# Kernel optimization log

Hardware: AMD Instinct MI355X
Metric: run time of the kernel (lower is better)

## Reference

```python
import jax, jax.numpy as jnp
import numpy as np

IN_SHAPE = 8192
OUT_SHAPE = 32
BATCH = 16384


def setup_inputs() -> dict:
    key = jax.random.key(0)
    kx, kw = jax.random.split(key)
    x = jax.random.normal(kx, (BATCH, IN_SHAPE), dtype=jnp.float32)
    # matches torch init: (rand*2-1)*0.001 -> uniform(-0.001, 0.001)
    weight = jax.random.uniform(kw, (OUT_SHAPE, IN_SHAPE), dtype=jnp.float32,
                                minval=-0.001, maxval=0.001)
    return {"x": x, "weight": weight}


def _binarize(weight):
    # scale = mean(|W|), detached
    scale = jax.lax.stop_gradient(jnp.mean(jnp.abs(weight)))
    clipped = jnp.clip(weight, -1.0, 1.0)
    # STE: forward value = scale*sign(W); gradient flows through clipped W
    return jax.lax.stop_gradient(scale * jnp.sign(weight) - clipped) + clipped


def reference(x, weight):
    bw = _binarize(weight)            # [out, in]
    return x @ bw.T                   # [batch, out]
```

## Files before the change

### kernel.cpp

```cpp
#include <hip/hip_runtime.h>

#define BATCH 16384
#define KDIM  8192
#define ODIM  32
#define SK    8
#define KSLICE (KDIM / SK)
#define KHALF  (KSLICE / 2)
#define KT    32
#define NT    (KHALF / KT)
#define THREADS 256

typedef short bf16x8 __attribute__((ext_vector_type(8)));
typedef float f32x16 __attribute__((ext_vector_type(16)));

__global__ void prep_kernel(const float* __restrict__ w,
                            unsigned short* __restrict__ bwTo,
                            float* __restrict__ partial) {
    int idx = blockIdx.x * 256 + threadIdx.x;
    float v = w[idx];
    bwTo[idx] = (v > 0.f) ? 0x3F80u : ((v < 0.f) ? 0xBF80u : 0u);

    float a = fabsf(v);
    #pragma unroll
    for (int off = 32; off; off >>= 1) a += __shfl_down(a, off, 64);
    __shared__ float red[4];
    int lane = threadIdx.x & 63, wv = threadIdx.x >> 6;
    if (lane == 0) red[wv] = a;
    __syncthreads();
    if (threadIdx.x == 0)
        partial[blockIdx.x] = (red[0] + red[1]) + (red[2] + red[3]);
}

__global__ __launch_bounds__(THREADS, 6)
void main_kernel(const float* __restrict__ x,
                 const unsigned short* __restrict__ bwTo,
                 float* __restrict__ pout) {
    __shared__ union {
        float buf[4][2][32][KT];
        float part[2][64][33];
    } sm;

    const int tid  = threadIdx.x;
    const int wv   = __builtin_amdgcn_readfirstlane(tid >> 6);
    const int lane = tid & 63;
    const int l31  = lane & 31, lhi = lane >> 5;
    const int kH   = wv & 1;
    const int rH   = wv >> 1;
    const int kb   = blockIdx.x & 7;
    const int rb   = blockIdx.x >> 3;
    const size_t rowbase = (size_t)rb * 64;
    const int kbase = kb * KSLICE + kH * KHALF;

    const int srow8 = lane >> 3;
    const int sc    = lane & 7;
    const int ssl   = sc ^ srow8;
    const float* __restrict__ g0 =
        x + (rowbase + rH * 32 + srow8) * (size_t)KDIM + kbase + 4 * sc;
    const float* __restrict__ g1 = g0 + (size_t)8  * KDIM;
    const float* __restrict__ g2 = g0 + (size_t)16 * KDIM;
    const float* __restrict__ g3 = g0 + (size_t)24 * KDIM;

    const unsigned short* __restrict__ bp =
        bwTo + (size_t)l31 * KDIM + kbase + lhi * 8;

    const int m7 = l31 & 7;
    const int ro00 = 4 * ((0 + 2 * lhi) ^ m7);
    const int ro01 = 4 * ((1 + 2 * lhi) ^ m7);
    const int ro10 = 4 * ((4 + 2 * lhi) ^ m7);
    const int ro11 = 4 * ((5 + 2 * lhi) ^ m7);
    const float* const rb0 = &sm.buf[wv][0][l31][0];
    const float* const rb1 = &sm.buf[wv][1][l31][0];

    f32x16 acc;
    #pragma unroll
    for (int i = 0; i < 16; ++i) acc[i] = 0.f;

    float4 st0, st1, st2, st3;
#define LOADT(t) do {                               \
        st0 = *(const float4*)(g0 + (t) * KT);      \
        st1 = *(const float4*)(g1 + (t) * KT);      \
        st2 = *(const float4*)(g2 + (t) * KT);      \
        st3 = *(const float4*)(g3 + (t) * KT);      \
    } while (0)
#define WRITET(db) do {                                         \
        *(float4*)&sm.buf[wv][db][srow8     ][4 * ssl] = st0;   \
        *(float4*)&sm.buf[wv][db][srow8 +  8][4 * ssl] = st1;   \
        *(float4*)&sm.buf[wv][db][srow8 + 16][4 * ssl] = st2;   \
        *(float4*)&sm.buf[wv][db][srow8 + 24][4 * ssl] = st3;   \
    } while (0)

    bf16x8 ahi, alo;
#define STEP(base, o0, o1, bfr) do {                                      \
        const float4 xa = *(const float4*)((base) + (o0));                \
        const float4 xb = *(const float4*)((base) + (o1));                \
        const float xf[8] = {xa.x, xa.y, xa.z, xa.w,                      \
                             xb.x, xb.y, xb.z, xb.w};                     \
        _Pragma("unroll")                                                 \
        for (int j = 0; j < 8; ++j) {                                     \
            unsigned bu = __float_as_uint(xf[j]);                         \
            float lo = xf[j] - __uint_as_float(bu & 0xFFFF0000u);         \
            ahi[j] = (short)(bu >> 16);                                   \
            alo[j] = (short)(__float_as_uint(lo) >> 16);                  \
        }                                                                 \
        acc = __builtin_amdgcn_mfma_f32_32x32x16_bf16(ahi, bfr, acc, 0, 0, 0); \
        acc = __builtin_amdgcn_mfma_f32_32x32x16_bf16(alo, bfr, acc, 0, 0, 0); \
    } while (0)

    LOADT(0);
    WRITET(0);
    LOADT(1);
    bf16x8 b0 = *(const bf16x8*)(bp);
    bf16x8 b1 = *(const bf16x8*)(bp + 16);

    for (int t = 0; t < NT; ++t) {
        const int db = t & 1;
        const float* base = db ? rb1 : rb0;

        STEP(base, ro00, ro01, b0);

        bf16x8 bn0, bn1;
        if (t + 1 < NT) {
            bn0 = *(const bf16x8*)(bp + (t + 1) * KT);
            bn1 = *(const bf16x8*)(bp + (t + 1) * KT + 16);
        }

        STEP(base, ro10, ro11, b1);

        if (t + 1 < NT) WRITET(db ^ 1);
        if (t + 2 < NT) LOADT(t + 2);
        b0 = bn0; b1 = bn1;
    }
#undef LOADT
#undef WRITET
#undef STEP

    __syncthreads();
    #pragma unroll
    for (int r = 0; r < 16; ++r) {
        int row32 = (r & 3) + 8 * (r >> 2) + 4 * lhi;
        sm.part[kH][rH * 32 + row32][l31] = acc[r];
    }
    __syncthreads();

    float* __restrict__ pb = pout + ((size_t)kb * BATCH + rowbase) * ODIM;
    #pragma unroll
    for (int i = 0; i < 8; ++i) {
        int j = tid + THREADS * i;
        int r = j >> 5, o = j & 31;
        pb[j] = sm.part[0][r][o] + sm.part[1][r][o];
    }
}

__global__ void reduce_kernel(const float* __restrict__ pout,
                              const float* __restrict__ partial,
                              float* __restrict__ out) {
    const int t = threadIdx.x;
    float a = (partial[t] + partial[t + 256]) + (partial[t + 512] + partial[t + 768]);
    #pragma unroll
    for (int off = 32; off; off >>= 1) a += __shfl_down(a, off, 64);
    __shared__ float red[4];
    __shared__ float sbc;
    if ((t & 63) == 0) red[t >> 6] = a;
    __syncthreads();
    if (t == 0)
        sbc = ((red[0] + red[1]) + (red[2] + red[3])) / (float)(ODIM * KDIM);
    __syncthreads();
    const float s = sbc;

    const int STRIDE = BATCH * ODIM / 4;
    int i = blockIdx.x * 256 + t;
    const float4* p = (const float4*)pout;
    float4 r = p[i];
    #pragma unroll
    for (int k = 1; k < SK; ++k) {
        float4 A = p[i + k * STRIDE];
        r.x += A.x; r.y += A.y; r.z += A.z; r.w += A.w;
    }
    r.x *= s; r.y *= s; r.z *= s; r.w *= s;
    ((float4*)out)[i] = r;
}

extern "C" void kernel_launch(void* const* d_in, const int* in_sizes, int n_in,
                              void* d_out, int out_size, void* d_ws, size_t ws_size,
                              hipStream_t stream) {
    const float* x = (const float*)d_in[0];
    const float* w = (const float*)d_in[1];
    float* out = (float*)d_out;

    float* wsf = (float*)d_ws;
    float* partial       = wsf;
    unsigned short* bwTo = (unsigned short*)(wsf + 1024);
    float* pout          = wsf + 1024 + (ODIM * KDIM / 2);

    prep_kernel<<<1024, 256, 0, stream>>>(w, bwTo, partial);
    main_kernel<<<256 * SK, THREADS, 0, stream>>>(x, bwTo, pout);
    reduce_kernel<<<BATCH * ODIM / 4 / 256, 256, 0, stream>>>(pout, partial, out);
}
```

Baseline: 126.5 us.

## Round x to single bf16 at load, store bf16 tiles in LDS, widen K tile

Replaces the split hi/lo bf16 emulation of fp32 (two MFMAs per step) with a single round-to-nearest bf16 conversion done at global-load time, so LDS holds bf16 instead of fp32 and each step issues one MFMA. The K tile doubles to 64 with a new swizzle, the B fragments are loaded directly per step rather than prefetched, and launch bounds drop to 5 waves. This halves MFMA work and LDS traffic but cuts x precision to bf16, which may break accuracy tolerance against the fp32 reference.

```diff
diff --git a/kernel.cpp b/kernel.cpp
--- a/kernel.cpp
+++ b/kernel.cpp
@@ -6,12 +6,21 @@
 #define SK    8
 #define KSLICE (KDIM / SK)
 #define KHALF  (KSLICE / 2)
-#define KT    32
+#define KT    64
 #define NT    (KHALF / KT)
 #define THREADS 256
 
 typedef short bf16x8 __attribute__((ext_vector_type(8)));
 typedef float f32x16 __attribute__((ext_vector_type(16)));
+
+__device__ __forceinline__ uint2 pack_bf16rn(float4 v) {
+    unsigned b0 = __float_as_uint(v.x), b1 = __float_as_uint(v.y);
+    unsigned b2 = __float_as_uint(v.z), b3 = __float_as_uint(v.w);
+    uint2 r;
+    r.x = ((b0 + 0x8000u) >> 16) | ((b1 + 0x8000u) & 0xFFFF0000u);
+    r.y = ((b2 + 0x8000u) >> 16) | ((b3 + 0x8000u) & 0xFFFF0000u);
+    return r;
+}
 
 __global__ void prep_kernel(const float* __restrict__ w,
                             unsigned short* __restrict__ bwTo,
@@ -31,12 +40,12 @@
         partial[blockIdx.x] = (red[0] + red[1]) + (red[2] + red[3]);
 }
 
-__global__ __launch_bounds__(THREADS, 6)
+__global__ __launch_bounds__(THREADS, 5)
 void main_kernel(const float* __restrict__ x,
                  const unsigned short* __restrict__ bwTo,
                  float* __restrict__ pout) {
     __shared__ union {
-        float buf[4][2][32][KT];
+        unsigned short buf[4][2][32][KT];
         float part[2][64][33];
     } sm;
 
@@ -44,6 +53,7 @@
     const int wv   = __builtin_amdgcn_readfirstlane(tid >> 6);
     const int lane = tid & 63;
     const int l31  = lane & 31, lhi = lane >> 5;
+    const int m7   = l31 & 7;
     const int kH   = wv & 1;
     const int rH   = wv >> 1;
     const int kb   = blockIdx.x & 7;
@@ -51,86 +61,77 @@
     const size_t rowbase = (size_t)rb * 64;
     const int kbase = kb * KSLICE + kH * KHALF;
 
-    const int srow8 = lane >> 3;
-    const int sc    = lane & 7;
-    const int ssl   = sc ^ srow8;
-    const float* __restrict__ g0 =
-        x + (rowbase + rH * 32 + srow8) * (size_t)KDIM + kbase + 4 * sc;
-    const float* __restrict__ g1 = g0 + (size_t)8  * KDIM;
-    const float* __restrict__ g2 = g0 + (size_t)16 * KDIM;
-    const float* __restrict__ g3 = g0 + (size_t)24 * KDIM;
+    const int srow4 = lane >> 4;
+    const int sc    = lane & 15;
+    const float* __restrict__ gb =
+        x + (rowbase + rH * 32 + srow4) * (size_t)KDIM + kbase + 4 * sc;
+
+    const int chE = (((sc >> 1) ^ srow4) << 3) + (sc & 1) * 4;
+    const int chO = chE ^ 32;
 
     const unsigned short* __restrict__ bp =
         bwTo + (size_t)l31 * KDIM + kbase + lhi * 8;
 
-    const int m7 = l31 & 7;
-    const int ro00 = 4 * ((0 + 2 * lhi) ^ m7);
-    const int ro01 = 4 * ((1 + 2 * lhi) ^ m7);
-    const int ro10 = 4 * ((4 + 2 * lhi) ^ m7);
-    const int ro11 = 4 * ((5 + 2 * lhi) ^ m7);
-    const float* const rb0 = &sm.buf[wv][0][l31][0];
-    const float* const rb1 = &sm.buf[wv][1][l31][0];
+    const int ro0 = l31 * 64 + (((0 + lhi) ^ m7) << 3);
+    const int ro1 = l31 * 64 + (((2 + lhi) ^ m7) << 3);
+    const int ro2 = l31 * 64 + (((4 + lhi) ^ m7) << 3);
+    const int ro3 = l31 * 64 + (((6 + lhi) ^ m7) << 3);
+    const unsigned short* const rbA = &sm.buf[wv][0][0][0];
+    const unsigned short* const rbB = &sm.buf[wv][1][0][0];
 
     f32x16 acc;
     #pragma unroll
     for (int i = 0; i < 16; ++i) acc[i] = 0.f;
 
-    float4 st0, st1, st2, st3;
-#define LOADT(t) do {                               \
-        st0 = *(const float4*)(g0 + (t) * KT);      \
-        st1 = *(const float4*)(g1 + (t) * KT);      \
-        st2 = *(const float4*)(g2 + (t) * KT);      \
-        st3 = *(const float4*)(g3 + (t) * KT);      \
-    } while (0)
-#define WRITET(db) do {                                         \
-        *(float4*)&sm.buf[wv][db][srow8     ][4 * ssl] = st0;   \
-        *(float4*)&sm.buf[wv][db][srow8 +  8][4 * ssl] = st1;   \
-        *(float4*)&sm.buf[wv][db][srow8 + 16][4 * ssl] = st2;   \
-        *(float4*)&sm.buf[wv][db][srow8 + 24][4 * ssl] = st3;   \
+    uint2 pk0, pk1, pk2, pk3, pk4, pk5, pk6, pk7;
+
+#define LOADPACK(t) do {                                                      \
+        float4 s0 = *(const float4*)(gb + (size_t) 0 * KDIM + (t) * KT);      \
+        float4 s1 = *(const float4*)(gb + (size_t) 4 * KDIM + (t) * KT);      \
+        float4 s2 = *(const float4*)(gb + (size_t) 8 * KDIM + (t) * KT);      \
+        float4 s3 = *(const float4*)(gb + (size_t)12 * KDIM + (t) * KT);      \
+        pk0 = pack_bf16rn(s0); pk1 = pack_bf16rn(s1);                         \
+        pk2 = pack_bf16rn(s2); pk3 = pack_bf16rn(s3);                         \
+        float4 s4 = *(const float4*)(gb + (size_t)16 * KDIM + (t) * KT);      \
+        float4 s5 = *(const float4*)(gb + (size_t)20 * KDIM + (t) * KT);      \
+        float4 s6 = *(const float4*)(gb + (size_t)24 * KDIM + (t) * KT);      \
+        float4 s7 = *(const float4*)(gb + (size_t)28 * KDIM + (t) * KT);      \
+        pk4 = pack_bf16rn(s4); pk5 = pack_bf16rn(s5);                         \
+        pk6 = pack_bf16rn(s6); pk7 = pack_bf16rn(s7);                         \
     } while (0)
 
-    bf16x8 ahi, alo;
-#define STEP(base, o0, o1, bfr) do {                                      \
-        const float4 xa = *(const float4*)((base) + (o0));                \
-        const float4 xb = *(const float4*)((base) + (o1));                \
-        const float xf[8] = {xa.x, xa.y, xa.z, xa.w,                      \
-                             xb.x, xb.y, xb.z, xb.w};                     \
-        _Pragma("unroll")                                                 \
-        for (int j = 0; j < 8; ++j) {                                     \
-            unsigned bu = __float_as_uint(xf[j]);                         \
-            float lo = xf[j] - __uint_as_float(bu & 0xFFFF0000u);         \
-            ahi[j] = (short)(bu >> 16);                                   \
-            alo[j] = (short)(__float_as_uint(lo) >> 16);                  \
-        }                                                                 \
-        acc = __builtin_amdgcn_mfma_f32_32x32x16_bf16(ahi, bfr, acc, 0, 0, 0); \
-        acc = __builtin_amdgcn_mfma_f32_32x32x16_bf16(alo, bfr, acc, 0, 0, 0); \
+#define WRITET(db) do {                                                       \
+        *(uint2*)&sm.buf[wv][db][ 0 + srow4][chE] = pk0;                      \
+        *(uint2*)&sm.buf[wv][db][ 4 + srow4][chO] = pk1;                      \
+        *(uint2*)&sm.buf[wv][db][ 8 + srow4][chE] = pk2;                      \
+        *(uint2*)&sm.buf[wv][db][12 + srow4][chO] = pk3;                      \
+        *(uint2*)&sm.buf[wv][db][16 + srow4][chE] = pk4;                      \
+        *(uint2*)&sm.buf[wv][db][20 + srow4][chO] = pk5;                      \
+        *(uint2*)&sm.buf[wv][db][24 + srow4][chE] = pk6;                      \
+        *(uint2*)&sm.buf[wv][db][28 + srow4][chO] = pk7;                      \
     } while (0)
 
-    LOADT(0);
+#define STEP(base, ro, boff) do {                                             \
+        bf16x8 av = *(const bf16x8*)((base) + (ro));                          \
+        bf16x8 bv = *(const bf16x8*)(bp + (boff));                            \
+        acc = __builtin_amdgcn_mfma_f32_32x32x16_bf16(av, bv, acc, 0, 0, 0);  \
+    } while (0)
+
+    LOADPACK(0);
     WRITET(0);
-    LOADT(1);
-    bf16x8 b0 = *(const bf16x8*)(bp);
-    bf16x8 b1 = *(const bf16x8*)(bp + 16);
+    LOADPACK(1);
 
     for (int t = 0; t < NT; ++t) {
-        const int db = t & 1;
-        const float* base = db ? rb1 : rb0;
-
-        STEP(base, ro00, ro01, b0);
-
-        bf16x8 bn0, bn1;
-        if (t + 1 < NT) {
-            bn0 = *(const bf16x8*)(bp + (t + 1) * KT);
-            bn1 = *(const bf16x8*)(bp + (t + 1) * KT + 16);
-        }
-
-        STEP(base, ro10, ro11, b1);
-
-        if (t + 1 < NT) WRITET(db ^ 1);
-        if (t + 2 < NT) LOADT(t + 2);
-        b0 = bn0; b1 = bn1;
+        const unsigned short* base = (t & 1) ? rbB : rbA;
+        const int tb = t * KT;
+        STEP(base, ro0, tb);
+        STEP(base, ro1, tb + 16);
+        STEP(base, ro2, tb + 32);
+        STEP(base, ro3, tb + 48);
+        if (t + 1 < NT) WRITET((t + 1) & 1);
+        if (t + 2 < NT) LOADPACK(t + 2);
     }
-#undef LOADT
+#undef LOADPACK
 #undef WRITET
 #undef STEP
 
```

Measured after the change: 126.5 us. Within noise of the previous version (-0.0%).
